# Kernel optimization log

Measured on AMD Instinct MI355X. Metric: run time of the kernel, lower is better.

The kernel has to match this reference:

```python
import jax, jax.numpy as jnp
import numpy as np

N = 50000
E = 800000
D_IN = 96
D_OUT = 128


def setup_inputs() -> dict:
    key = jax.random.key(0)
    k1, k2, k3, k4, k5 = jax.random.split(key, 5)
    x = jax.random.normal(k1, (N, D_IN), dtype=jnp.float32)
    edge_index = jax.random.randint(k2, (2, E), 0, N, dtype=jnp.int32)
    s = 1.0 / np.sqrt(D_IN)
    # lin_l: applied to aggregated neighbor features (has bias in PyG SAGEConv)
    W_l = jax.random.uniform(k3, (D_OUT, D_IN), jnp.float32, -s, s)
    b_l = jax.random.uniform(k4, (D_OUT,), jnp.float32, -s, s)
    # lin_r: root/self weight (no bias)
    W_r = jax.random.uniform(k5, (D_OUT, D_IN), jnp.float32, -s, s)
    return {"x": x, "edge_index": edge_index, "W_l": W_l, "b_l": b_l, "W_r": W_r}


def reference(x, edge_index, W_l, b_l, W_r):
    src, dst = edge_index[0], edge_index[1]
    # gather source features, mean-aggregate onto targets
    msg = x[src]  # [E, D_IN]
    summed = jax.ops.segment_sum(msg, dst, num_segments=N)  # [N, D_IN]
    count = jax.ops.segment_sum(jnp.ones((E,), x.dtype), dst, num_segments=N)
    agg = summed / jnp.maximum(count, 1.0)[:, None]
    # SAGEConv: lin_l(agg) + lin_r(x), then layer-level ReLU
    out = agg @ W_l.T + b_l + x @ W_r.T
    return jax.nn.relu(out)
```

## Files before the change

kernel.cpp:

```cpp
#include <hip/hip_runtime.h>
#include <hip/hip_bf16.h>

#define N_NODES 50000
#define N_EDGES 800000
#define D_IN 96
#define D_OUT 128
#define CAP 64
#define CAPP 72

#define NPB 64
#define N_BINS ((N_NODES + NPB - 1) / NPB)
#define CAP_SUB 24
#define PART_EPB 3125
#define PART_BLOCKS (N_EDGES / PART_EPB)
#define PART_SLOTS 13

#define CONV_THREADS (N_NODES * 12)
#define CONV_BLOCKS ((CONV_THREADS + 255) / 256)
#define WCONV_BLOCKS 12

#define AG_BLOCKS N_BINS
#define AH_PITCH 104

typedef unsigned short u16;
typedef __attribute__((ext_vector_type(8))) short short8;
typedef __attribute__((ext_vector_type(4))) float f32x4;

__device__ __forceinline__ u16 f2bf(float f) {
    unsigned u = __float_as_uint(f);
    unsigned r = (u + 0x7FFFu + ((u >> 16) & 1u)) >> 16;
    return (u16)r;
}
__device__ __forceinline__ float bf2f(u16 h) {
    return __uint_as_float(((unsigned)h) << 16);
}

__global__ __launch_bounds__(256) void sage_part_conv(
    const int* __restrict__ src,
    const int* __restrict__ dst,
    const float* __restrict__ x,
    const float* __restrict__ Wl,
    const float* __restrict__ Wr,
    u16* __restrict__ cnts,
    unsigned* __restrict__ binbuf,
    u16* __restrict__ xh,
    u16* __restrict__ Wfrag)
{
    __shared__ unsigned hist[N_BINS];
    __shared__ unsigned cur[N_BINS];

    const int b = blockIdx.x;
    const int tid = (int)threadIdx.x;

    if (b < PART_BLOCKS) {
        for (int i = tid; i < N_BINS; i += 256) { hist[i] = 0u; cur[i] = 0u; }
        __syncthreads();

        const int ebase = b * PART_EPB;
        const int e0 = ebase + tid;
        int d[PART_SLOTS], s[PART_SLOTS];
#pragma unroll
        for (int i = 0; i < PART_SLOTS; i++) {
            int valid = (tid + i * 256) < PART_EPB;
            int e = valid ? (e0 + i * 256) : ebase;
            d[i] = dst[e];
            s[i] = src[e];
        }
#pragma unroll
        for (int i = 0; i < PART_SLOTS; i++) {
            if ((tid + i * 256) < PART_EPB)
                atomicAdd(&hist[d[i] >> 6], 1u);
        }
        __syncthreads();
        for (int i = tid; i < N_BINS; i += 256)
            cnts[(size_t)i * PART_BLOCKS + b] = (u16)hist[i];
#pragma unroll
        for (int i = 0; i < PART_SLOTS; i++) {
            if ((tid + i * 256) < PART_EPB) {
                int bn = d[i] >> 6;
                unsigned dl = (unsigned)(d[i] & 63);
                unsigned loc = atomicAdd(&cur[bn], 1u);
                if (loc < CAP_SUB)
                    binbuf[((unsigned)bn * PART_BLOCKS + (unsigned)b) * CAP_SUB
                           + loc] = (dl << 16) | (unsigned)s[i];
            }
        }
    } else if (b < PART_BLOCKS + CONV_BLOCKS) {
        unsigned t = (unsigned)(b - PART_BLOCKS) * 256u + threadIdx.x;
        if (t >= (unsigned)CONV_THREADS) return;
        unsigned n = t / 12u;
        unsigned c8 = t - n * 12u;
        const float* p = x + (size_t)n * D_IN + c8 * 8u;
        short8 v;
#pragma unroll
        for (int i = 0; i < 8; i++) v[i] = (short)f2bf(p[i]);
        *(short8*)(xh + (size_t)n * D_IN + c8 * 8u) = v;
    } else {
        int idx = (b - PART_BLOCKS - CONV_BLOCKS) * 256 + tid;
        int j = idx / 24;
        int c8 = idx - j * 24;
        int kc = c8 >> 2;
        int quad = c8 & 3;
        const float* wsrc = (c8 < 12) ? (Wl + (size_t)j * D_IN + c8 * 8)
                                      : (Wr + (size_t)j * D_IN + (c8 - 12) * 8);
        int jt = j >> 4;
        int col = j & 15;
        short8 v;
#pragma unroll
        for (int i = 0; i < 8; i++) v[i] = (short)f2bf(wsrc[i]);
        *(short8*)(Wfrag + (((jt * 6 + kc) * 64) + col + 16 * quad) * 8) = v;
    }
}

__global__ __launch_bounds__(512) void sage_agg_gemm(
    const u16* __restrict__ xh,
    const u16* __restrict__ cnts,
    const unsigned* __restrict__ binbuf,
    const u16* __restrict__ Wfrag,
    const float* __restrict__ bl,
    float* __restrict__ out)
{
    __shared__ __align__(16) u16 bkt[NPB * CAPP];
    __shared__ unsigned cnt_l[NPB];
    __shared__ __align__(16) u16 Ah[NPB * AH_PITCH];

    const int j = blockIdx.x;
    const int tid = (int)threadIdx.x;
    const int n0 = j * NPB;

    if (tid < NPB) cnt_l[tid] = 0u;
    __syncthreads();

    if (tid < PART_BLOCKS) {
        unsigned cnt_t = cnts[(size_t)j * PART_BLOCKS + tid];
        const uint4* sc = (const uint4*)(binbuf
                          + ((size_t)j * PART_BLOCKS + tid) * CAP_SUB);
        unsigned lim = cnt_t < CAP_SUB ? cnt_t : CAP_SUB;
        uint4 q0 = {0,0,0,0}, q1 = {0,0,0,0}, q2 = {0,0,0,0};
        uint4 q3 = {0,0,0,0}, q4 = {0,0,0,0}, q5 = {0,0,0,0};
        if (lim > 0)  q0 = sc[0];
        if (lim > 4)  q1 = sc[1];
        if (lim > 8)  q2 = sc[2];
        if (lim > 12) q3 = sc[3];
        if (lim > 16) q4 = sc[4];
        if (lim > 20) q5 = sc[5];
        unsigned buf[CAP_SUB];
        buf[0]=q0.x;  buf[1]=q0.y;  buf[2]=q0.z;  buf[3]=q0.w;
        buf[4]=q1.x;  buf[5]=q1.y;  buf[6]=q1.z;  buf[7]=q1.w;
        buf[8]=q2.x;  buf[9]=q2.y;  buf[10]=q2.z; buf[11]=q2.w;
        buf[12]=q3.x; buf[13]=q3.y; buf[14]=q3.z; buf[15]=q3.w;
        buf[16]=q4.x; buf[17]=q4.y; buf[18]=q4.z; buf[19]=q4.w;
        buf[20]=q5.x; buf[21]=q5.y; buf[22]=q5.z; buf[23]=q5.w;
#pragma unroll
        for (int e = 0; e < CAP_SUB; e++) {
            if ((unsigned)e < lim) {
                unsigned w = buf[e];
                unsigned r = w >> 16;
                unsigned p = atomicAdd(&cnt_l[r], 1u);
                if (p < CAP) bkt[r * CAPP + p] = (u16)(w & 0xFFFFu);
            }
        }
    }
    __syncthreads();

#pragma unroll
    for (int rep = 0; rep < 3; rep++) {
        int pair = rep * 256 + (tid >> 1);
        int m = pair / 12;
        int c8 = pair - m * 12;
        int half = tid & 1;
        int n = n0 + m;

        float acc[8];
#pragma unroll
        for (int i = 0; i < 8; i++) acc[i] = 0.0f;
        int deg = 0;

        if (n < N_NODES) {
            deg = (int)cnt_l[m];
            int dc = deg < CAP ? deg : CAP;
            int mid = ((dc >> 1) + 4) & ~7;
            int e_lo = half ? mid : 0;
            int e_hi = half ? dc : mid;
            const u16* brow = bkt + m * CAPP;
            int e = e_lo;
            for (; e + 8 <= e_hi; e += 8) {
                short8 id = *(const short8*)(brow + e);
                short8 v[8];
#pragma unroll
                for (int q = 0; q < 8; q++) {
                    unsigned s = (u16)id[q];
                    v[q] = *(const short8*)(xh + s * (unsigned)D_IN + c8 * 8u);
                }
#pragma unroll
                for (int q = 0; q < 8; q++)
#pragma unroll
                    for (int i = 0; i < 8; i++) acc[i] += bf2f((u16)v[q][i]);
            }
            if (e + 4 <= e_hi) {
                unsigned s0 = brow[e + 0];
                unsigned s1 = brow[e + 1];
                unsigned s2 = brow[e + 2];
                unsigned s3 = brow[e + 3];
                short8 v0 = *(const short8*)(xh + s0 * (unsigned)D_IN + c8 * 8u);
                short8 v1 = *(const short8*)(xh + s1 * (unsigned)D_IN + c8 * 8u);
                short8 v2 = *(const short8*)(xh + s2 * (unsigned)D_IN + c8 * 8u);
                short8 v3 = *(const short8*)(xh + s3 * (unsigned)D_IN + c8 * 8u);
#pragma unroll
                for (int i = 0; i < 8; i++)
                    acc[i] += bf2f((u16)v0[i]) + bf2f((u16)v1[i])
                            + bf2f((u16)v2[i]) + bf2f((u16)v3[i]);
                e += 4;
            }
            for (; e < e_hi; e++) {
                unsigned s = brow[e];
                short8 v = *(const short8*)(xh + s * (unsigned)D_IN + c8 * 8u);
#pragma unroll
                for (int i = 0; i < 8; i++) acc[i] += bf2f((u16)v[i]);
            }
        }

#pragma unroll
        for (int i = 0; i < 8; i++)
            acc[i] += __shfl_xor(acc[i], 1);

        if (half == 0) {
            float invd = (n < N_NODES) ? 1.0f / fmaxf((float)deg, 1.0f) : 0.0f;
            short8 o;
#pragma unroll
            for (int i = 0; i < 8; i++)
                o[i] = (short)f2bf(acc[i] * invd);
            *(short8*)(Ah + m * AH_PITCH + c8 * 8) = o;
        }
    }
    __syncthreads();

    const int wave = tid >> 6;
    const int lane = tid & 63;
    const int m16 = lane & 15;
    const int quad = lane >> 4;
    const int tile = wave & 3;
    const int jt0 = (wave >> 2) * 4;
    const int tilebase = n0 + tile * 16;
    if (tilebase >= N_NODES) return;

    int nn = tilebase + m16;
    nn = nn < N_NODES ? nn : N_NODES - 1;

    const u16* arow = Ah + (tile * 16 + m16) * AH_PITCH + quad * 8;
    const u16* xrow = xh + (size_t)nn * D_IN + quad * 8;
    short8 a[6];
#pragma unroll
    for (int kc = 0; kc < 3; kc++) a[kc]     = *(const short8*)(arow + kc * 32);
#pragma unroll
    for (int kc = 0; kc < 3; kc++) a[3 + kc] = *(const short8*)(xrow + kc * 32);

#pragma unroll
    for (int jt = 0; jt < 4; jt++) {
        const int jtt = jt0 + jt;
        f32x4 acc = {0.0f, 0.0f, 0.0f, 0.0f};
#pragma unroll
        for (int kc = 0; kc < 6; kc++) {
            short8 bfrag = *(const short8*)(Wfrag + ((jtt * 6 + kc) * 64 + lane) * 8);
            acc = __builtin_amdgcn_mfma_f32_16x16x32_bf16(a[kc], bfrag, acc, 0, 0, 0);
        }
        const int jj = jtt * 16 + m16;
        const float bj = bl[jj];
#pragma unroll
        for (int r = 0; r < 4; r++) {
            int row = quad * 4 + r;
            int n = tilebase + row;
            if (n < N_NODES)
                out[(size_t)n * D_OUT + jj] = fmaxf(acc[r] + bj, 0.0f);
        }
    }
}

extern "C" void kernel_launch(void* const* d_in, const int* in_sizes, int n_in,
                              void* d_out, int out_size, void* d_ws, size_t ws_size,
                              hipStream_t stream) {
    const float* x   = (const float*)d_in[0];
    const int* eidx  = (const int*)d_in[1];
    const float* Wl  = (const float*)d_in[2];
    const float* bl  = (const float*)d_in[3];
    const float* Wr  = (const float*)d_in[4];
    float* out = (float*)d_out;

    const int* src = eidx;
    const int* dst = eidx + N_EDGES;

    char* ws = (char*)d_ws;
    unsigned* binbuf = (unsigned*)ws;
    u16*      cnts   = (u16*)(ws + 19218432);
    u16*      xh     = (u16*)(ws + 19618816);
    u16*      Wfrag  = (u16*)(ws + 29218816);

    {
        dim3 grid(PART_BLOCKS + CONV_BLOCKS + WCONV_BLOCKS);
        sage_part_conv<<<grid, 256, 0, stream>>>(src, dst, x, Wl, Wr,
                                                 cnts, binbuf, xh, Wfrag);
    }
    {
        dim3 grid(AG_BLOCKS);
        sage_agg_gemm<<<grid, 512, 0, stream>>>(xh, cnts, binbuf, Wfrag, bl, out);
    }
}
```

Baseline: 127.6 us.

## Split bf16 features into two half-width arrays and pad bin buffer stride

The bf16 copy of x is stored as two separate arrays of 48 columns each. The aggregation is reordered so the first 768 tasks of a block gather only from the low half and the remaining tasks gather from the high half. This shrinks the working set each half of the gather touches at a time, aiming for better L2 locality of the random row gathers. The per-bin sub-buffer stride is also padded from 24 to 32 words so each segment starts aligned. The cost is more workspace and extra address selection logic, including in the GEMM A-fragment load.

```diff
diff --git a/kernel.cpp b/kernel.cpp
--- a/kernel.cpp
+++ b/kernel.cpp
@@ -11,6 +11,7 @@
 #define NPB 64
 #define N_BINS ((N_NODES + NPB - 1) / NPB)
 #define CAP_SUB 24
+#define CAP_STRIDE 32
 #define PART_EPB 3125
 #define PART_BLOCKS (N_EDGES / PART_EPB)
 #define PART_SLOTS 13
@@ -21,6 +22,7 @@
 
 #define AG_BLOCKS N_BINS
 #define AH_PITCH 104
+#define DH 48
 
 typedef unsigned short u16;
 typedef __attribute__((ext_vector_type(8))) short short8;
@@ -43,7 +45,8 @@
     const float* __restrict__ Wr,
     u16* __restrict__ cnts,
     unsigned* __restrict__ binbuf,
-    u16* __restrict__ xh,
+    u16* __restrict__ xh_lo,
+    u16* __restrict__ xh_hi,
     u16* __restrict__ Wfrag)
 {
     __shared__ unsigned hist[N_BINS];
@@ -81,7 +84,7 @@
                 unsigned dl = (unsigned)(d[i] & 63);
                 unsigned loc = atomicAdd(&cur[bn], 1u);
                 if (loc < CAP_SUB)
-                    binbuf[((unsigned)bn * PART_BLOCKS + (unsigned)b) * CAP_SUB
+                    binbuf[((unsigned)bn * PART_BLOCKS + (unsigned)b) * CAP_STRIDE
                            + loc] = (dl << 16) | (unsigned)s[i];
             }
         }
@@ -94,7 +97,9 @@
         short8 v;
 #pragma unroll
         for (int i = 0; i < 8; i++) v[i] = (short)f2bf(p[i]);
-        *(short8*)(xh + (size_t)n * D_IN + c8 * 8u) = v;
+        u16* dp = (c8 < 6) ? (xh_lo + (size_t)n * DH + c8 * 8u)
+                           : (xh_hi + (size_t)n * DH + (c8 - 6) * 8u);
+        *(short8*)dp = v;
     } else {
         int idx = (b - PART_BLOCKS - CONV_BLOCKS) * 256 + tid;
         int j = idx / 24;
@@ -113,7 +118,8 @@
 }
 
 __global__ __launch_bounds__(512) void sage_agg_gemm(
-    const u16* __restrict__ xh,
+    const u16* __restrict__ xh_lo,
+    const u16* __restrict__ xh_hi,
     const u16* __restrict__ cnts,
     const unsigned* __restrict__ binbuf,
     const u16* __restrict__ Wfrag,
@@ -134,7 +140,7 @@
     if (tid < PART_BLOCKS) {
         unsigned cnt_t = cnts[(size_t)j * PART_BLOCKS + tid];
         const uint4* sc = (const uint4*)(binbuf
-                          + ((size_t)j * PART_BLOCKS + tid) * CAP_SUB);
+                          + ((size_t)j * PART_BLOCKS + tid) * CAP_STRIDE);
         unsigned lim = cnt_t < CAP_SUB ? cnt_t : CAP_SUB;
         uint4 q0 = {0,0,0,0}, q1 = {0,0,0,0}, q2 = {0,0,0,0};
         uint4 q3 = {0,0,0,0}, q4 = {0,0,0,0}, q5 = {0,0,0,0};
@@ -165,11 +171,16 @@
 
 #pragma unroll
     for (int rep = 0; rep < 3; rep++) {
-        int pair = rep * 256 + (tid >> 1);
-        int m = pair / 12;
-        int c8 = pair - m * 12;
-        int half = tid & 1;
+        int task = rep * 512 + tid;
+        int s = task >= 768 ? 1 : 0;
+        int t2 = task - s * 768;
+        int m = t2 / 12;
+        int rem = t2 - m * 12;
+        int c8l = rem >> 1;
+        int half = rem & 1;
+        int c8 = s * 6 + c8l;
         int n = n0 + m;
+        const u16* xbase = s ? xh_hi : xh_lo;
 
         float acc[8];
 #pragma unroll
@@ -189,8 +200,8 @@
                 short8 v[8];
 #pragma unroll
                 for (int q = 0; q < 8; q++) {
-                    unsigned s = (u16)id[q];
-                    v[q] = *(const short8*)(xh + s * (unsigned)D_IN + c8 * 8u);
+                    unsigned sidx = (u16)id[q];
+                    v[q] = *(const short8*)(xbase + sidx * (unsigned)DH + c8l * 8u);
                 }
 #pragma unroll
                 for (int q = 0; q < 8; q++)
@@ -202,10 +213,10 @@
                 unsigned s1 = brow[e + 1];
                 unsigned s2 = brow[e + 2];
                 unsigned s3 = brow[e + 3];
-                short8 v0 = *(const short8*)(xh + s0 * (unsigned)D_IN + c8 * 8u);
-                short8 v1 = *(const short8*)(xh + s1 * (unsigned)D_IN + c8 * 8u);
-                short8 v2 = *(const short8*)(xh + s2 * (unsigned)D_IN + c8 * 8u);
-                short8 v3 = *(const short8*)(xh + s3 * (unsigned)D_IN + c8 * 8u);
+                short8 v0 = *(const short8*)(xbase + s0 * (unsigned)DH + c8l * 8u);
+                short8 v1 = *(const short8*)(xbase + s1 * (unsigned)DH + c8l * 8u);
+                short8 v2 = *(const short8*)(xbase + s2 * (unsigned)DH + c8l * 8u);
+                short8 v3 = *(const short8*)(xbase + s3 * (unsigned)DH + c8l * 8u);
 #pragma unroll
                 for (int i = 0; i < 8; i++)
                     acc[i] += bf2f((u16)v0[i]) + bf2f((u16)v1[i])
@@ -213,8 +224,8 @@
                 e += 4;
             }
             for (; e < e_hi; e++) {
-                unsigned s = brow[e];
-                short8 v = *(const short8*)(xh + s * (unsigned)D_IN + c8 * 8u);
+                unsigned sidx = brow[e];
+                short8 v = *(const short8*)(xbase + sidx * (unsigned)DH + c8l * 8u);
 #pragma unroll
                 for (int i = 0; i < 8; i++) acc[i] += bf2f((u16)v[i]);
             }
@@ -248,12 +259,16 @@
     nn = nn < N_NODES ? nn : N_NODES - 1;
 
     const u16* arow = Ah + (tile * 16 + m16) * AH_PITCH + quad * 8;
-    const u16* xrow = xh + (size_t)nn * D_IN + quad * 8;
     short8 a[6];
 #pragma unroll
-    for (int kc = 0; kc < 3; kc++) a[kc]     = *(const short8*)(arow + kc * 32);
-#pragma unroll
-    for (int kc = 0; kc < 3; kc++) a[3 + kc] = *(const short8*)(xrow + kc * 32);
+    for (int kc = 0; kc < 3; kc++) a[kc] = *(const short8*)(arow + kc * 32);
+#pragma unroll
+    for (int kc = 0; kc < 3; kc++) {
+        int off = kc * 32 + quad * 8;
+        const u16* p = (off < DH) ? (xh_lo + (size_t)nn * DH + off)
+                                  : (xh_hi + (size_t)nn * DH + (off - DH));
+        a[3 + kc] = *(const short8*)p;
+    }
 
 #pragma unroll
     for (int jt = 0; jt < 4; jt++) {
@@ -291,17 +306,19 @@
 
     char* ws = (char*)d_ws;
     unsigned* binbuf = (unsigned*)ws;
-    u16*      cnts   = (u16*)(ws + 19218432);
-    u16*      xh     = (u16*)(ws + 19618816);
-    u16*      Wfrag  = (u16*)(ws + 29218816);
+    u16*      cnts   = (u16*)(ws + 25624576);
+    u16*      xh_lo  = (u16*)(ws + 26025088);
+    u16*      xh_hi  = (u16*)(ws + 30825088);
+    u16*      Wfrag  = (u16*)(ws + 35625088);
 
     {
         dim3 grid(PART_BLOCKS + CONV_BLOCKS + WCONV_BLOCKS);
         sage_part_conv<<<grid, 256, 0, stream>>>(src, dst, x, Wl, Wr,
-                                                 cnts, binbuf, xh, Wfrag);
+                                                 cnts, binbuf, xh_lo, xh_hi, Wfrag);
     }
     {
         dim3 grid(AG_BLOCKS);
-        sage_agg_gemm<<<grid, 512, 0, stream>>>(xh, cnts, binbuf, Wfrag, bl, out);
-    }
-}
+        sage_agg_gemm<<<grid, 512, 0, stream>>>(xh_lo, xh_hi, cnts, binbuf,
+                                                Wfrag, bl, out);
+    }
+}
```

Result: slower. 134.4 us (+5.3%).

## Split each node's neighbor list by source half to localize gathers

Applied to the files above, without the earlier changes.

Edges in each partition cell are now separated by whether the source index falls in the lower or upper half of the node range. Low-half sources fill the cell from the front and high-half sources from the back, with packed counts. The aggregation kernel keeps two sub-buckets per node and walks the low-source neighbors before the high-source ones, so concurrent gathers stay within a smaller region of xh for better cache locality. In exchange the partition phase does more work: extra branches, extra atomics and a padded cell stride (32 instead of 24) that enlarges binbuf. Per-half caps of 32 could also drop neighbors that the previous single cap of 64 kept.

```diff
diff --git a/kernel.cpp b/kernel.cpp
--- a/kernel.cpp
+++ b/kernel.cpp
@@ -7,10 +7,13 @@
 #define D_OUT 128
 #define CAP 64
 #define CAPP 72
+#define HALF_CAP 32
+#define N_HALF 25000
 
 #define NPB 64
 #define N_BINS ((N_NODES + NPB - 1) / NPB)
 #define CAP_SUB 24
+#define CAP_STRIDE 32
 #define PART_EPB 3125
 #define PART_BLOCKS (N_EDGES / PART_EPB)
 #define PART_SLOTS 13
@@ -34,6 +37,45 @@
 __device__ __forceinline__ float bf2f(u16 h) {
     return __uint_as_float(((unsigned)h) << 16);
 }
+
+#define WALK(e0, e1, brow, xbase, c8, acc)                                     \
+    {                                                                          \
+        int e = (e0);                                                          \
+        for (; e + 8 <= (e1); e += 8) {                                        \
+            short8 id = *(const short8*)((brow) + e);                          \
+            short8 v[8];                                                       \
+            _Pragma("unroll")                                                  \
+            for (int q = 0; q < 8; q++) {                                      \
+                unsigned s = (u16)id[q];                                       \
+                v[q] = *(const short8*)((xbase) + s * (unsigned)D_IN + (c8) * 8u); \
+            }                                                                  \
+            _Pragma("unroll")                                                  \
+            for (int q = 0; q < 8; q++)                                        \
+                _Pragma("unroll")                                              \
+                for (int i = 0; i < 8; i++) (acc)[i] += bf2f((u16)v[q][i]);    \
+        }                                                                      \
+        if (e + 4 <= (e1)) {                                                   \
+            unsigned s0 = (brow)[e + 0];                                       \
+            unsigned s1 = (brow)[e + 1];                                       \
+            unsigned s2 = (brow)[e + 2];                                       \
+            unsigned s3 = (brow)[e + 3];                                       \
+            short8 v0 = *(const short8*)((xbase) + s0 * (unsigned)D_IN + (c8) * 8u); \
+            short8 v1 = *(const short8*)((xbase) + s1 * (unsigned)D_IN + (c8) * 8u); \
+            short8 v2 = *(const short8*)((xbase) + s2 * (unsigned)D_IN + (c8) * 8u); \
+            short8 v3 = *(const short8*)((xbase) + s3 * (unsigned)D_IN + (c8) * 8u); \
+            _Pragma("unroll")                                                  \
+            for (int i = 0; i < 8; i++)                                        \
+                (acc)[i] += bf2f((u16)v0[i]) + bf2f((u16)v1[i])                \
+                          + bf2f((u16)v2[i]) + bf2f((u16)v3[i]);               \
+            e += 4;                                                            \
+        }                                                                      \
+        for (; e < (e1); e++) {                                                \
+            unsigned s = (brow)[e];                                            \
+            short8 v = *(const short8*)((xbase) + s * (unsigned)D_IN + (c8) * 8u); \
+            _Pragma("unroll")                                                  \
+            for (int i = 0; i < 8; i++) (acc)[i] += bf2f((u16)v[i]);           \
+        }                                                                      \
+    }
 
 __global__ __launch_bounds__(256) void sage_part_conv(
     const int* __restrict__ src,
@@ -46,14 +88,16 @@
     u16* __restrict__ xh,
     u16* __restrict__ Wfrag)
 {
-    __shared__ unsigned hist[N_BINS];
-    __shared__ unsigned cur[N_BINS];
+    __shared__ unsigned hist_lo[N_BINS], hist_hi[N_BINS];
+    __shared__ unsigned cur_lo[N_BINS],  cur_hi[N_BINS];
 
     const int b = blockIdx.x;
     const int tid = (int)threadIdx.x;
 
     if (b < PART_BLOCKS) {
-        for (int i = tid; i < N_BINS; i += 256) { hist[i] = 0u; cur[i] = 0u; }
+        for (int i = tid; i < N_BINS; i += 256) {
+            hist_lo[i] = 0u; hist_hi[i] = 0u; cur_lo[i] = 0u; cur_hi[i] = 0u;
+        }
         __syncthreads();
 
         const int ebase = b * PART_EPB;
@@ -68,21 +112,33 @@
         }
 #pragma unroll
         for (int i = 0; i < PART_SLOTS; i++) {
-            if ((tid + i * 256) < PART_EPB)
-                atomicAdd(&hist[d[i] >> 6], 1u);
+            if ((tid + i * 256) < PART_EPB) {
+                int bn = d[i] >> 6;
+                if (s[i] < N_HALF) atomicAdd(&hist_lo[bn], 1u);
+                else               atomicAdd(&hist_hi[bn], 1u);
+            }
         }
         __syncthreads();
-        for (int i = tid; i < N_BINS; i += 256)
-            cnts[(size_t)i * PART_BLOCKS + b] = (u16)hist[i];
+        for (int i = tid; i < N_BINS; i += 256) {
+            unsigned hl = hist_lo[i] > CAP_SUB ? CAP_SUB : hist_lo[i];
+            unsigned hh = hist_hi[i] > CAP_SUB ? CAP_SUB : hist_hi[i];
+            cnts[(size_t)i * PART_BLOCKS + b] = (u16)((hl << 8) | hh);
+        }
 #pragma unroll
         for (int i = 0; i < PART_SLOTS; i++) {
             if ((tid + i * 256) < PART_EPB) {
                 int bn = d[i] >> 6;
                 unsigned dl = (unsigned)(d[i] & 63);
-                unsigned loc = atomicAdd(&cur[bn], 1u);
-                if (loc < CAP_SUB)
-                    binbuf[((unsigned)bn * PART_BLOCKS + (unsigned)b) * CAP_SUB
-                           + loc] = (dl << 16) | (unsigned)s[i];
+                unsigned w = (dl << 16) | (unsigned)s[i];
+                unsigned cell = ((unsigned)bn * PART_BLOCKS + (unsigned)b)
+                                * CAP_STRIDE;
+                if (s[i] < N_HALF) {
+                    unsigned loc = atomicAdd(&cur_lo[bn], 1u);
+                    if (loc < CAP_SUB) binbuf[cell + loc] = w;
+                } else {
+                    unsigned loc = atomicAdd(&cur_hi[bn], 1u);
+                    if (loc < CAP_SUB) binbuf[cell + (CAP_SUB - 1u - loc)] = w;
+                }
             }
         }
     } else if (b < PART_BLOCKS + CONV_BLOCKS) {
@@ -121,29 +177,30 @@
     float* __restrict__ out)
 {
     __shared__ __align__(16) u16 bkt[NPB * CAPP];
-    __shared__ unsigned cnt_l[NPB];
+    __shared__ unsigned cnt_lo_l[NPB], cnt_hi_l[NPB];
     __shared__ __align__(16) u16 Ah[NPB * AH_PITCH];
 
     const int j = blockIdx.x;
     const int tid = (int)threadIdx.x;
     const int n0 = j * NPB;
 
-    if (tid < NPB) cnt_l[tid] = 0u;
+    if (tid < NPB) { cnt_lo_l[tid] = 0u; cnt_hi_l[tid] = 0u; }
     __syncthreads();
 
     if (tid < PART_BLOCKS) {
-        unsigned cnt_t = cnts[(size_t)j * PART_BLOCKS + tid];
+        unsigned pk = cnts[(size_t)j * PART_BLOCKS + tid];
+        unsigned cl = (pk >> 8) & 0xFFu; if (cl > CAP_SUB) cl = CAP_SUB;
+        unsigned ch = pk & 0xFFu;        if (ch > CAP_SUB) ch = CAP_SUB;
         const uint4* sc = (const uint4*)(binbuf
-                          + ((size_t)j * PART_BLOCKS + tid) * CAP_SUB);
-        unsigned lim = cnt_t < CAP_SUB ? cnt_t : CAP_SUB;
+                          + ((size_t)j * PART_BLOCKS + tid) * CAP_STRIDE);
         uint4 q0 = {0,0,0,0}, q1 = {0,0,0,0}, q2 = {0,0,0,0};
         uint4 q3 = {0,0,0,0}, q4 = {0,0,0,0}, q5 = {0,0,0,0};
-        if (lim > 0)  q0 = sc[0];
-        if (lim > 4)  q1 = sc[1];
-        if (lim > 8)  q2 = sc[2];
-        if (lim > 12) q3 = sc[3];
-        if (lim > 16) q4 = sc[4];
-        if (lim > 20) q5 = sc[5];
+        if (cl > 0  || ch > 20) q0 = sc[0];
+        if (cl > 4  || ch > 16) q1 = sc[1];
+        if (cl > 8  || ch > 12) q2 = sc[2];
+        if (cl > 12 || ch > 8)  q3 = sc[3];
+        if (cl > 16 || ch > 4)  q4 = sc[4];
+        if (cl > 20 || ch > 0)  q5 = sc[5];
         unsigned buf[CAP_SUB];
         buf[0]=q0.x;  buf[1]=q0.y;  buf[2]=q0.z;  buf[3]=q0.w;
         buf[4]=q1.x;  buf[5]=q1.y;  buf[6]=q1.z;  buf[7]=q1.w;
@@ -153,11 +210,18 @@
         buf[20]=q5.x; buf[21]=q5.y; buf[22]=q5.z; buf[23]=q5.w;
 #pragma unroll
         for (int e = 0; e < CAP_SUB; e++) {
-            if ((unsigned)e < lim) {
+            bool is_lo = (unsigned)e < cl;
+            bool is_hi = (unsigned)e >= (CAP_SUB - ch);
+            if (is_lo) {
                 unsigned w = buf[e];
                 unsigned r = w >> 16;
-                unsigned p = atomicAdd(&cnt_l[r], 1u);
-                if (p < CAP) bkt[r * CAPP + p] = (u16)(w & 0xFFFFu);
+                unsigned p = atomicAdd(&cnt_lo_l[r], 1u);
+                if (p < HALF_CAP) bkt[r * CAPP + p] = (u16)(w & 0xFFFFu);
+            } else if (is_hi) {
+                unsigned w = buf[e];
+                unsigned r = w >> 16;
+                unsigned p = atomicAdd(&cnt_hi_l[r], 1u);
+                if (p < HALF_CAP) bkt[r * CAPP + HALF_CAP + p] = (u16)(w & 0xFFFFu);
             }
         }
     }
@@ -174,49 +238,23 @@
         float acc[8];
 #pragma unroll
         for (int i = 0; i < 8; i++) acc[i] = 0.0f;
-        int deg = 0;
+        int cl = 0, ch = 0;
 
         if (n < N_NODES) {
-            deg = (int)cnt_l[m];
-            int dc = deg < CAP ? deg : CAP;
-            int mid = ((dc >> 1) + 4) & ~7;
-            int e_lo = half ? mid : 0;
-            int e_hi = half ? dc : mid;
+            cl = (int)cnt_lo_l[m]; if (cl > HALF_CAP) cl = HALF_CAP;
+            ch = (int)cnt_hi_l[m]; if (ch > HALF_CAP) ch = HALF_CAP;
             const u16* brow = bkt + m * CAPP;
-            int e = e_lo;
-            for (; e + 8 <= e_hi; e += 8) {
-                short8 id = *(const short8*)(brow + e);
-                short8 v[8];
-#pragma unroll
-                for (int q = 0; q < 8; q++) {
-                    unsigned s = (u16)id[q];
-                    v[q] = *(const short8*)(xh + s * (unsigned)D_IN + c8 * 8u);
-                }
-#pragma unroll
-                for (int q = 0; q < 8; q++)
-#pragma unroll
-                    for (int i = 0; i < 8; i++) acc[i] += bf2f((u16)v[q][i]);
-            }
-            if (e + 4 <= e_hi) {
-                unsigned s0 = brow[e + 0];
-                unsigned s1 = brow[e + 1];
-                unsigned s2 = brow[e + 2];
-                unsigned s3 = brow[e + 3];
-                short8 v0 = *(const short8*)(xh + s0 * (unsigned)D_IN + c8 * 8u);
-                short8 v1 = *(const short8*)(xh + s1 * (unsigned)D_IN + c8 * 8u);
-                short8 v2 = *(const short8*)(xh + s2 * (unsigned)D_IN + c8 * 8u);
-                short8 v3 = *(const short8*)(xh + s3 * (unsigned)D_IN + c8 * 8u);
-#pragma unroll
-                for (int i = 0; i < 8; i++)
-                    acc[i] += bf2f((u16)v0[i]) + bf2f((u16)v1[i])
-                            + bf2f((u16)v2[i]) + bf2f((u16)v3[i]);
-                e += 4;
-            }
-            for (; e < e_hi; e++) {
-                unsigned s = brow[e];
-                short8 v = *(const short8*)(xh + s * (unsigned)D_IN + c8 * 8u);
-#pragma unroll
-                for (int i = 0; i < 8; i++) acc[i] += bf2f((u16)v[i]);
+            {
+                int mid = ((cl >> 1) + 4) & ~7;
+                int es = half ? mid : 0;
+                int ee = half ? cl : mid;
+                WALK(es, ee, brow, xh, c8, acc)
+            }
+            {
+                int mid = ((ch >> 1) + 4) & ~7;
+                int es = HALF_CAP + (half ? mid : 0);
+                int ee = HALF_CAP + (half ? ch : mid);
+                WALK(es, ee, brow, xh, c8, acc)
             }
         }
 
@@ -225,7 +263,8 @@
             acc[i] += __shfl_xor(acc[i], 1);
 
         if (half == 0) {
-            float invd = (n < N_NODES) ? 1.0f / fmaxf((float)deg, 1.0f) : 0.0f;
+            float invd = (n < N_NODES)
+                       ? 1.0f / fmaxf((float)(cl + ch), 1.0f) : 0.0f;
             short8 o;
 #pragma unroll
             for (int i = 0; i < 8; i++)
@@ -291,9 +330,9 @@
 
     char* ws = (char*)d_ws;
     unsigned* binbuf = (unsigned*)ws;
-    u16*      cnts   = (u16*)(ws + 19218432);
-    u16*      xh     = (u16*)(ws + 19618816);
-    u16*      Wfrag  = (u16*)(ws + 29218816);
+    u16*      cnts   = (u16*)(ws + 25624576);
+    u16*      xh     = (u16*)(ws + 26025088);
+    u16*      Wfrag  = (u16*)(ws + 35625088);
 
     {
         dim3 grid(PART_BLOCKS + CONV_BLOCKS + WCONV_BLOCKS);
@@ -302,6 +341,7 @@
     }
     {
         dim3 grid(AG_BLOCKS);
-        sage_agg_gemm<<<grid, 512, 0, stream>>>(xh, cnts, binbuf, Wfrag, bl, out);
-    }
-}
+        sage_agg_gemm<<<grid, 512, 0, stream>>>(xh, cnts, binbuf,
+                                                Wfrag, bl, out);
+    }
+}
```

Measured after the change: 143.9 us. 12.8% more time.
